# Performance work log

Hardware: AMD Instinct MI355X
Metric: run time of the kernel (lower is better)

## Reference

```python
import jax, jax.numpy as jnp
import numpy as np

DIM = 64
HEADS = 4            # self.num_heads = 2 * num_heads(=2)
SMK = 5
KS = 7
EPS = 1e-5
SCALE = (DIM // HEADS) ** -0.5


def pool_mat(n, out=7):
    # AdaptiveAvgPool2d bin matrix: P[i, j] = 1/size if floor(i*n/out) <= j < ceil((i+1)*n/out)
    P = np.zeros((out, n), np.float32)
    for i in range(out):
        s = (i * n) // out
        e = -((-(i + 1) * n) // out)
        P[i, s:e] = 1.0 / (e - s)
    return jnp.asarray(P)


def bn(x, g, b, m, v):
    # inference BatchNorm2d on [B,C,H,W]
    return (x - m[:, None, None]) * (g[:, None, None] * jax.lax.rsqrt(v[:, None, None] + EPS)) + b[:, None, None]


def conv1x1(x, w):
    return jnp.einsum('oi,bihw->bohw', w, x)


def rpb_bias(rpb, H, W, k):
    # replicate apply_rpb gather indexing (incl. the flip over flattened HW)
    rs = 2 * k - 1
    ih0 = np.arange(k)
    idx_k = (ih0[:, None] * rs + ih0[None, :]).reshape(-1)        # [k*k]
    rh = np.ones(k, np.int64); rh[k // 2] = H - (k - 1)
    rw = np.ones(k, np.int64); rw[k // 2] = W - (k - 1)
    ih = np.repeat(ih0, rh)                                       # [H]
    iw = np.repeat(ih0, rw)                                       # [W]
    bias_hw = ih[:, None] * rs + iw[None, :]                      # [H,W]
    bias_idx = (bias_hw[..., None] + idx_k).reshape(-1, k * k)[::-1].copy()  # [H*W,k*k]
    flat = rpb.reshape(rpb.shape[0], -1)                          # [G, rs*rs]
    return flat[:, bias_idx].reshape(1, rpb.shape[0], H, W, k * k)


def na2d_av(attn, value, k):
    # NATTEN-style neighborhood AV: window start clamped to stay in-bounds
    B, G, H, W, _ = attn.shape
    si = np.clip(np.arange(H) - k // 2, 0, H - k)
    sj = np.clip(np.arange(W) - k // 2, 0, W - k)
    ii = si[:, None] + np.arange(k)    # [H,k]
    jj = sj[:, None] + np.arange(k)    # [W,k]
    v = value[:, :, ii][:, :, :, :, jj]         # [B,G,H,k,W,k,C]
    a = attn.reshape(B, G, H, W, k, k)
    return jnp.einsum('bghwij,bghiwjc->bghwc', a, v)


def reference(x, wq_w, wq_g, wq_b, wq_m, wq_v,
              wk_w, wk_g, wk_b, wk_m, wk_v,
              proj_w, proj_b, rpb1, rpb2,
              dy_w, dy_g, dy_b, dy_m, dy_v):
    B, C, H, W = x.shape
    G = HEADS
    q, kctx = jnp.split(x, 2, axis=1)                      # [B,C/2,H,W] each
    q = bn(conv1x1(q, wq_w), wq_g, wq_b, wq_m, wq_v) * SCALE
    Ph, Pw = pool_mat(H), pool_mat(W)
    kp = jnp.einsum('ph,bchw,qw->bcpq', Ph, kctx, Pw)      # adaptive avg pool to 7x7
    k = bn(conv1x1(kp, wk_w), wk_g, wk_b, wk_m, wk_v)
    q = q.reshape(B, G, -1, H * W)                          # b g c n
    k = k.reshape(B, G, -1, 49)                             # b g c l
    w = jnp.einsum('bgcn,bgcl->bgnl', q, k)
    w = w.transpose(0, 3, 1, 2)                             # b l g n
    w = jnp.einsum('ol,blgn->bogn', proj_w, w) + proj_b[None, :, None, None]  # b (74) g n
    w = w.transpose(0, 2, 3, 1).reshape(B, G, H, W, SMK * SMK + KS * KS)
    attn1 = w[..., :SMK * SMK]
    attn2 = w[..., SMK * SMK:]
    attn1 = jax.nn.softmax(attn1 + rpb_bias(rpb1, H, W, SMK), axis=-1)
    attn2 = jax.nn.softmax(attn2 + rpb_bias(rpb2, H, W, KS), axis=-1)
    c = C // (2 * G)
    value = x.reshape(B, 2, G, c, H, W).transpose(1, 0, 2, 4, 5, 3)  # m b g h w c
    x1 = na2d_av(attn1, value[0], SMK)
    x2 = na2d_av(attn2, value[1], KS)
    out = jnp.concatenate([x1, x2], axis=1)                 # b (2g) h w c
    out = out.transpose(0, 1, 4, 2, 3).reshape(B, C, H, W)  # b (g c) h w
    return bn(conv1x1(out, dy_w), dy_g, dy_b, dy_m, dy_v)


def setup_inputs() -> dict:
    key = jax.random.key(0)
    ks = jax.random.split(key, 20)
    h = DIM // 2
    def bnp(k):
        k1, k2, k3, k4 = jax.random.split(k, 4)
        return (jax.random.uniform(k1, (0,)),)  # unused
    inp = {
        'x': jax.random.normal(ks[0], (8, DIM, 64, 64), jnp.float32),
        'wq_w': jax.random.normal(ks[1], (h, h), jnp.float32) * (h ** -0.5),
        'wq_g': jax.random.uniform(ks[2], (h,), jnp.float32, 0.5, 1.5),
        'wq_b': jax.random.normal(ks[3], (h,), jnp.float32) * 0.1,
        'wq_m': jax.random.normal(ks[4], (h,), jnp.float32) * 0.1,
        'wq_v': jax.random.uniform(ks[5], (h,), jnp.float32, 0.5, 1.5),
        'wk_w': jax.random.normal(ks[6], (h, h), jnp.float32) * (h ** -0.5),
        'wk_g': jax.random.uniform(ks[7], (h,), jnp.float32, 0.5, 1.5),
        'wk_b': jax.random.normal(ks[8], (h,), jnp.float32) * 0.1,
        'wk_m': jax.random.normal(ks[9], (h,), jnp.float32) * 0.1,
        'wk_v': jax.random.uniform(ks[10], (h,), jnp.float32, 0.5, 1.5),
        'proj_w': jax.random.normal(ks[11], (SMK * SMK + KS * KS, 49), jnp.float32) * (49 ** -0.5),
        'proj_b': jax.random.normal(ks[12], (SMK * SMK + KS * KS,), jnp.float32) * 0.02,
        'rpb1': jax.random.normal(ks[13], (HEADS, 2 * SMK - 1, 2 * SMK - 1), jnp.float32) * 0.02,
        'rpb2': jax.random.normal(ks[14], (HEADS, 2 * KS - 1, 2 * KS - 1), jnp.float32) * 0.02,
        'dy_w': jax.random.normal(ks[15], (DIM, DIM), jnp.float32) * (DIM ** -0.5),
        'dy_g': jax.random.uniform(ks[16], (DIM,), jnp.float32, 0.5, 1.5),
        'dy_b': jax.random.normal(ks[17], (DIM,), jnp.float32) * 0.1,
        'dy_m': jax.random.normal(ks[18], (DIM,), jnp.float32) * 0.1,
        'dy_v': jax.random.uniform(ks[19], (DIM,), jnp.float32, 0.5, 1.5),
    }
    return inp
```

## Files before the change

kernel.cpp:

```cpp
#include <hip/hip_runtime.h>

#define EPSV 1e-5f

#define OFF_W    12544
#define OFF_WQT  31488
#define OFF_DYT  32512

typedef float f4u __attribute__((ext_vector_type(4), aligned(4)));

__global__ __launch_bounds__(256) void pool_prep_kernel(
    const float* __restrict__ x,
    const float* __restrict__ wk_w, const float* __restrict__ wk_g,
    const float* __restrict__ wk_b, const float* __restrict__ wk_m,
    const float* __restrict__ wk_v,
    const float* __restrict__ wq_w, const float* __restrict__ dy_w,
    float* __restrict__ ws)
{
  const int bid = blockIdx.x;
  const int tid = threadIdx.x;

  if (bid >= 56) {
    const int t = (bid - 56) * 256 + tid;
    float* wqT = ws + OFF_WQT;
    float* dyT = ws + OFF_DYT;
    if (t < 1024) {
      const int i = t >> 5, o = t & 31;
      wqT[t] = wq_w[o * 32 + i];
    } else {
      const int t2 = t - 1024;
      const int i = t2 >> 6, o = t2 & 63;
      dyT[t2] = dy_w[o * 64 + i];
    }
    return;
  }

  float* kbuf = ws;
  const int b = bid / 7;
  const int p = bid % 7;
  __shared__ float s_tmp[32 * 64];
  __shared__ float s_kp[32 * 7];

  const int sh = (p * 64) / 7, eh = ((p + 1) * 64 + 6) / 7;
  const float invH = 1.0f / (float)(eh - sh);
  for (int idx = tid; idx < 2048; idx += 256) {
    const int c = idx >> 6, ww = idx & 63;
    const float* xp = x + ((size_t)(b * 64 + 32 + c)) * 4096 + ww;
    float s = 0.f;
    for (int hh = sh; hh < eh; ++hh) s += xp[hh * 64];
    s_tmp[idx] = s * invH;
  }
  __syncthreads();
  if (tid < 224) {
    const int c = tid / 7, q = tid % 7;
    const int sw = (q * 64) / 7, ew = ((q + 1) * 64 + 6) / 7;
    float s = 0.f;
    for (int ww = sw; ww < ew; ++ww) s += s_tmp[c * 64 + ww];
    s_kp[c * 7 + q] = s / (float)(ew - sw);
  }
  __syncthreads();
  if (tid < 224) {
    const int o = tid / 7, q = tid % 7;
    float s = 0.f;
#pragma unroll
    for (int i = 0; i < 32; i++) s += wk_w[o * 32 + i] * s_kp[i * 7 + q];
    const float sc = wk_g[o] * rsqrtf(wk_v[o] + EPSV);
    const int g = o >> 3, c = o & 7, l = p * 7 + q;
    kbuf[(((size_t)b * 4 + g) * 8 + c) * 49 + l] =
        (s - wk_m[o]) * sc + wk_b[o];
  }
}

__global__ __launch_bounds__(256) void fold_w_kernel(
    const float* __restrict__ proj_w, const float* __restrict__ ws_in,
    float* __restrict__ Wout)
{
  const int bg = blockIdx.x;
  const int tid = threadIdx.x;
  __shared__ float s_k[392];
  for (int i = tid; i < 392; i += 256) s_k[i] = ws_in[(size_t)bg * 392 + i];
  __syncthreads();
  for (int idx = tid; idx < 592; idx += 256) {
    const int o = idx >> 3, c = idx & 7;
    float s = 0.f;
#pragma unroll
    for (int l = 0; l < 49; l++) s += proj_w[o * 49 + l] * s_k[c * 49 + l];
    Wout[(size_t)bg * 592 + idx] = s;
  }
}

__global__ __launch_bounds__(512, 3) void contmix_main(
    const float* __restrict__ x,
    const float* __restrict__ wq_g, const float* __restrict__ wq_b,
    const float* __restrict__ wq_m, const float* __restrict__ wq_v,
    const float* __restrict__ proj_b,
    const float* __restrict__ rpb1, const float* __restrict__ rpb2,
    const float* __restrict__ dy_g, const float* __restrict__ dy_b,
    const float* __restrict__ dy_m, const float* __restrict__ dy_v,
    const float* __restrict__ ws,
    float* __restrict__ out)
{
  __shared__ float s_rpb1[4 * 81];
  __shared__ float s_rpb2[4 * 169];
  __shared__ float s_val[64 * 64];
  __shared__ float s_q[32 * 64];

  const int bx = blockIdx.x;
  const int b = bx >> 6;
  const int h = bx & 63;
  const int tid = threadIdx.x;
  const int w = tid & 63;
  const int bru = __builtin_amdgcn_readfirstlane(tid >> 8);
  const int gu  = __builtin_amdgcn_readfirstlane((tid >> 6) & 3);

  for (int i = tid; i < 324; i += 512) s_rpb1[i] = rpb1[i];
  for (int i = tid; i < 676; i += 512) s_rpb2[i] = rpb2[i];

  const float* xb = x + (size_t)b * 64 * 4096;

  float q8[8];
  if (bru == 0) {
#pragma unroll
    for (int o = 0; o < 8; o++) q8[o] = 0.f;
    const float* wqt = ws + OFF_WQT + gu * 8;
#pragma unroll
    for (int i = 0; i < 32; i++) {
      const float xv = xb[i * 4096 + h * 64 + w];
#pragma unroll
      for (int o = 0; o < 8; o++) q8[o] += wqt[i * 32 + o] * xv;
    }
#pragma unroll
    for (int o = 0; o < 8; o++) {
      const int oc = gu * 8 + o;
      const float s = wq_g[oc] * rsqrtf(wq_v[oc] + EPSV);
      q8[o] = (q8[o] * s + (wq_b[oc] - wq_m[oc] * s)) * 0.25f;
      s_q[(gu * 8 + o) * 64 + w] = q8[o];
    }
  }
  __syncthreads();
  if (bru != 0) {
#pragma unroll
    for (int o = 0; o < 8; o++) q8[o] = s_q[(gu * 8 + o) * 64 + w];
  }

  const float* Wr = ws + OFF_W + (size_t)(b * 4 + gu) * 592;

  const int ph = 63 - h, pw = 63 - w;

  if (bru == 0) {
    const int bih5 = ph - min(max(ph - 2, 0), 59);
    const int biw5 = pw - min(max(pw - 2, 0), 59);
    const int si5 = min(max(h - 2, 0), 59), sj5 = min(max(w - 2, 0), 59);
    float l1[25];
#pragma unroll
    for (int o = 0; o < 25; o++) {
      const float* wo = Wr + o * 8;
      float s = proj_b[o];
#pragma unroll
      for (int c = 0; c < 8; c++) s += wo[c] * q8[c];
      l1[o] = s;
    }
    const float* rp1 = s_rpb1 + gu * 81 + bih5 * 9 + biw5;
#pragma unroll
    for (int ki = 0; ki < 5; ki++)
#pragma unroll
      for (int kj = 0; kj < 5; kj++) l1[ki * 5 + kj] += rp1[ki * 9 + kj];

    float mx = l1[0];
#pragma unroll
    for (int o = 1; o < 25; o++) mx = fmaxf(mx, l1[o]);
    float sum = 0.f;
#pragma unroll
    for (int o = 0; o < 25; o++) {
      const float e = __expf(l1[o] - mx);
      l1[o] = e;
      sum += e;
    }
    const float inv = 1.f / sum;

    float acc[8];
#pragma unroll
    for (int c = 0; c < 8; c++) acc[c] = 0.f;
    const float* vb = xb + gu * 8 * 4096;
#pragma unroll
    for (int i = 0; i < 5; i++) {
      const float a0 = l1[i * 5 + 0], a1 = l1[i * 5 + 1], a2 = l1[i * 5 + 2];
      const float a3 = l1[i * 5 + 3], a4 = l1[i * 5 + 4];
      const float* vr0 = vb + (si5 + i) * 64 + sj5;
#pragma unroll
      for (int c = 0; c < 8; c++) {
        const float* vr = vr0 + c * 4096;
        const f4u f = *(const f4u*)vr;
        const float v4 = vr[4];
        acc[c] += a0 * f.x + a1 * f.y + a2 * f.z + a3 * f.w + a4 * v4;
      }
    }
#pragma unroll
    for (int c = 0; c < 8; c++) s_val[(gu * 8 + c) * 64 + w] = acc[c] * inv;
  } else {
    const int bih7 = ph - min(max(ph - 3, 0), 57);
    const int biw7 = pw - min(max(pw - 3, 0), 57);
    const int si7 = min(max(h - 3, 0), 57), sj7 = min(max(w - 3, 0), 57);
    float l2[49];
#pragma unroll
    for (int o = 0; o < 49; o++) {
      const float* wo = Wr + (25 + o) * 8;
      float s = proj_b[25 + o];
#pragma unroll
      for (int c = 0; c < 8; c++) s += wo[c] * q8[c];
      l2[o] = s;
    }
    const float* rp2 = s_rpb2 + gu * 169 + bih7 * 13 + biw7;
#pragma unroll
    for (int ki = 0; ki < 7; ki++)
#pragma unroll
      for (int kj = 0; kj < 7; kj++) l2[ki * 7 + kj] += rp2[ki * 13 + kj];

    float mx = l2[0];
#pragma unroll
    for (int o = 1; o < 49; o++) mx = fmaxf(mx, l2[o]);
    float sum = 0.f;
#pragma unroll
    for (int o = 0; o < 49; o++) {
      const float e = __expf(l2[o] - mx);
      l2[o] = e;
      sum += e;
    }
    const float inv = 1.f / sum;

    float acc[8];
#pragma unroll
    for (int c = 0; c < 8; c++) acc[c] = 0.f;
    const float* vb = xb + (32 + gu * 8) * 4096;
#pragma unroll
    for (int i = 0; i < 7; i++) {
      const float a0 = l2[i * 7 + 0], a1 = l2[i * 7 + 1], a2 = l2[i * 7 + 2];
      const float a3 = l2[i * 7 + 3], a4 = l2[i * 7 + 4], a5 = l2[i * 7 + 5];
      const float a6 = l2[i * 7 + 6];
      const float* vr0 = vb + (si7 + i) * 64 + sj7;
#pragma unroll
      for (int c = 0; c < 8; c++) {
        const float* vr = vr0 + c * 4096;
        const f4u fa = *(const f4u*)vr;
        const f4u fb = *(const f4u*)(vr + 3);
        acc[c] += a0 * fa.x + a1 * fa.y + a2 * fa.z + a3 * fa.w +
                  a4 * fb.y + a5 * fb.z + a6 * fb.w;
      }
    }
#pragma unroll
    for (int c = 0; c < 8; c++) s_val[(32 + gu * 8 + c) * 64 + w] = acc[c] * inv;
  }

  __syncthreads();

  {
    const int ogu = __builtin_amdgcn_readfirstlane(tid >> 6);
    float facc[8];
#pragma unroll
    for (int oo = 0; oo < 8; oo++) facc[oo] = 0.f;
    const float* dyt = ws + OFF_DYT + ogu * 8;
#pragma unroll
    for (int i = 0; i < 64; i++) {
      const float v = s_val[i * 64 + w];
#pragma unroll
      for (int oo = 0; oo < 8; oo++) facc[oo] += dyt[i * 64 + oo] * v;
    }
#pragma unroll
    for (int oo = 0; oo < 8; oo++) {
      const int oc = ogu * 8 + oo;
      const float sc = dy_g[oc] * rsqrtf(dy_v[oc] + EPSV);
      out[((size_t)(b * 64 + oc)) * 4096 + h * 64 + w] =
          (facc[oo] - dy_m[oc]) * sc + dy_b[oc];
    }
  }
}

extern "C" void kernel_launch(void* const* d_in, const int* in_sizes, int n_in,
                              void* d_out, int out_size, void* d_ws, size_t ws_size,
                              hipStream_t stream)
{
  const float* x      = (const float*)d_in[0];
  const float* wq_w   = (const float*)d_in[1];
  const float* wq_g   = (const float*)d_in[2];
  const float* wq_b   = (const float*)d_in[3];
  const float* wq_m   = (const float*)d_in[4];
  const float* wq_v   = (const float*)d_in[5];
  const float* wk_w   = (const float*)d_in[6];
  const float* wk_g   = (const float*)d_in[7];
  const float* wk_b   = (const float*)d_in[8];
  const float* wk_m   = (const float*)d_in[9];
  const float* wk_v   = (const float*)d_in[10];
  const float* proj_w = (const float*)d_in[11];
  const float* proj_b = (const float*)d_in[12];
  const float* rpb1   = (const float*)d_in[13];
  const float* rpb2   = (const float*)d_in[14];
  const float* dy_w   = (const float*)d_in[15];
  const float* dy_g   = (const float*)d_in[16];
  const float* dy_b   = (const float*)d_in[17];
  const float* dy_m   = (const float*)d_in[18];
  const float* dy_v   = (const float*)d_in[19];

  float* ws = (float*)d_ws;

  pool_prep_kernel<<<76, 256, 0, stream>>>(x, wk_w, wk_g, wk_b, wk_m, wk_v,
                                           wq_w, dy_w, ws);
  fold_w_kernel<<<32, 256, 0, stream>>>(proj_w, ws, ws + OFF_W);
  contmix_main<<<512, 512, 0, stream>>>(x, wq_g, wq_b, wq_m, wq_v,
                                        proj_b, rpb1, rpb2,
                                        dy_g, dy_b, dy_m, dy_v,
                                        ws, (float*)d_out);
}
```

Baseline: 170.0 us.

## Split fused attention kernel into per-branch blocks plus separate final conv

Splits the fused main kernel in two. The first kernel runs the 5x5 and 7x7 attention branches in separate 256-thread blocks (1024 blocks), each recomputing q from an LDS-staged x row, and writes the attended values to a global workspace buffer. The second kernel loads those values into LDS and applies the final 1x1 conv with BatchNorm. The goal is to remove load imbalance between the 25-tap and 49-tap branches within a block and to drop register pressure. The cost is an extra kernel launch, a global round trip for the intermediate values, and duplicated q computation.

```diff
diff --git a/kernel.cpp b/kernel.cpp
--- a/kernel.cpp
+++ b/kernel.cpp
@@ -5,6 +5,7 @@
 #define OFF_W    12544
 #define OFF_WQT  31488
 #define OFF_DYT  32512
+#define OFF_VAL  40960
 
 typedef float f4u __attribute__((ext_vector_type(4), aligned(4)));
 
@@ -88,43 +89,47 @@
   }
 }
 
-__global__ __launch_bounds__(512, 3) void contmix_main(
+__global__ __launch_bounds__(256) void attn_kernel(
     const float* __restrict__ x,
     const float* __restrict__ wq_g, const float* __restrict__ wq_b,
     const float* __restrict__ wq_m, const float* __restrict__ wq_v,
     const float* __restrict__ proj_b,
     const float* __restrict__ rpb1, const float* __restrict__ rpb2,
-    const float* __restrict__ dy_g, const float* __restrict__ dy_b,
-    const float* __restrict__ dy_m, const float* __restrict__ dy_v,
     const float* __restrict__ ws,
-    float* __restrict__ out)
-{
-  __shared__ float s_rpb1[4 * 81];
-  __shared__ float s_rpb2[4 * 169];
-  __shared__ float s_val[64 * 64];
-  __shared__ float s_q[32 * 64];
-
-  const int bx = blockIdx.x;
-  const int b = bx >> 6;
-  const int h = bx & 63;
+    float* __restrict__ vbuf)
+{
+  __shared__ float s_rpb[4 * 169];
+  __shared__ float s_xq[32 * 64];
+
+  const int bid = blockIdx.x;
+  const int br = bid & 1;
+  const int h = (bid >> 1) & 63;
+  const int b = bid >> 7;
   const int tid = threadIdx.x;
   const int w = tid & 63;
-  const int bru = __builtin_amdgcn_readfirstlane(tid >> 8);
-  const int gu  = __builtin_amdgcn_readfirstlane((tid >> 6) & 3);
-
-  for (int i = tid; i < 324; i += 512) s_rpb1[i] = rpb1[i];
-  for (int i = tid; i < 676; i += 512) s_rpb2[i] = rpb2[i];
+  const int gu = __builtin_amdgcn_readfirstlane(tid >> 6);
 
   const float* xb = x + (size_t)b * 64 * 4096;
 
+  for (int idx = tid; idx < 2048; idx += 256) {
+    const int c = idx >> 6, ww = idx & 63;
+    s_xq[idx] = xb[c * 4096 + h * 64 + ww];
+  }
+  if (br == 0) {
+    for (int i = tid; i < 324; i += 256) s_rpb[i] = rpb1[i];
+  } else {
+    for (int i = tid; i < 676; i += 256) s_rpb[i] = rpb2[i];
+  }
+  __syncthreads();
+
   float q8[8];
-  if (bru == 0) {
-#pragma unroll
-    for (int o = 0; o < 8; o++) q8[o] = 0.f;
+#pragma unroll
+  for (int o = 0; o < 8; o++) q8[o] = 0.f;
+  {
     const float* wqt = ws + OFF_WQT + gu * 8;
 #pragma unroll
     for (int i = 0; i < 32; i++) {
-      const float xv = xb[i * 4096 + h * 64 + w];
+      const float xv = s_xq[i * 64 + w];
 #pragma unroll
       for (int o = 0; o < 8; o++) q8[o] += wqt[i * 32 + o] * xv;
     }
@@ -133,20 +138,14 @@
       const int oc = gu * 8 + o;
       const float s = wq_g[oc] * rsqrtf(wq_v[oc] + EPSV);
       q8[o] = (q8[o] * s + (wq_b[oc] - wq_m[oc] * s)) * 0.25f;
-      s_q[(gu * 8 + o) * 64 + w] = q8[o];
-    }
-  }
-  __syncthreads();
-  if (bru != 0) {
-#pragma unroll
-    for (int o = 0; o < 8; o++) q8[o] = s_q[(gu * 8 + o) * 64 + w];
+    }
   }
 
   const float* Wr = ws + OFF_W + (size_t)(b * 4 + gu) * 592;
 
   const int ph = 63 - h, pw = 63 - w;
 
-  if (bru == 0) {
+  if (br == 0) {
     const int bih5 = ph - min(max(ph - 2, 0), 59);
     const int biw5 = pw - min(max(pw - 2, 0), 59);
     const int si5 = min(max(h - 2, 0), 59), sj5 = min(max(w - 2, 0), 59);
@@ -159,7 +158,7 @@
       for (int c = 0; c < 8; c++) s += wo[c] * q8[c];
       l1[o] = s;
     }
-    const float* rp1 = s_rpb1 + gu * 81 + bih5 * 9 + biw5;
+    const float* rp1 = s_rpb + gu * 81 + bih5 * 9 + biw5;
 #pragma unroll
     for (int ki = 0; ki < 5; ki++)
 #pragma unroll
@@ -195,7 +194,8 @@
       }
     }
 #pragma unroll
-    for (int c = 0; c < 8; c++) s_val[(gu * 8 + c) * 64 + w] = acc[c] * inv;
+    for (int c = 0; c < 8; c++)
+      vbuf[((size_t)(b * 64 + gu * 8 + c)) * 4096 + h * 64 + w] = acc[c] * inv;
   } else {
     const int bih7 = ph - min(max(ph - 3, 0), 57);
     const int biw7 = pw - min(max(pw - 3, 0), 57);
@@ -209,7 +209,7 @@
       for (int c = 0; c < 8; c++) s += wo[c] * q8[c];
       l2[o] = s;
     }
-    const float* rp2 = s_rpb2 + gu * 169 + bih7 * 13 + biw7;
+    const float* rp2 = s_rpb + gu * 169 + bih7 * 13 + biw7;
 #pragma unroll
     for (int ki = 0; ki < 7; ki++)
 #pragma unroll
@@ -247,30 +247,51 @@
       }
     }
 #pragma unroll
-    for (int c = 0; c < 8; c++) s_val[(32 + gu * 8 + c) * 64 + w] = acc[c] * inv;
-  }
-
-  __syncthreads();
-
-  {
-    const int ogu = __builtin_amdgcn_readfirstlane(tid >> 6);
-    float facc[8];
-#pragma unroll
-    for (int oo = 0; oo < 8; oo++) facc[oo] = 0.f;
-    const float* dyt = ws + OFF_DYT + ogu * 8;
-#pragma unroll
-    for (int i = 0; i < 64; i++) {
-      const float v = s_val[i * 64 + w];
-#pragma unroll
-      for (int oo = 0; oo < 8; oo++) facc[oo] += dyt[i * 64 + oo] * v;
-    }
-#pragma unroll
-    for (int oo = 0; oo < 8; oo++) {
-      const int oc = ogu * 8 + oo;
-      const float sc = dy_g[oc] * rsqrtf(dy_v[oc] + EPSV);
-      out[((size_t)(b * 64 + oc)) * 4096 + h * 64 + w] =
-          (facc[oo] - dy_m[oc]) * sc + dy_b[oc];
-    }
+    for (int c = 0; c < 8; c++)
+      vbuf[((size_t)(b * 64 + 32 + gu * 8 + c)) * 4096 + h * 64 + w] =
+          acc[c] * inv;
+  }
+}
+
+__global__ __launch_bounds__(512) void final_conv_kernel(
+    const float* __restrict__ vbuf,
+    const float* __restrict__ dy_g, const float* __restrict__ dy_b,
+    const float* __restrict__ dy_m, const float* __restrict__ dy_v,
+    const float* __restrict__ ws,
+    float* __restrict__ out)
+{
+  __shared__ float s_val[64 * 64];
+
+  const int bx = blockIdx.x;
+  const int b = bx >> 6;
+  const int h = bx & 63;
+  const int tid = threadIdx.x;
+  const int w = tid & 63;
+  const int ogu = __builtin_amdgcn_readfirstlane(tid >> 6);
+
+  for (int idx4 = tid; idx4 < 1024; idx4 += 512) {
+    const int ic = idx4 >> 4, w4 = idx4 & 15;
+    *(f4u*)&s_val[ic * 64 + w4 * 4] =
+        *(const f4u*)&vbuf[((size_t)(b * 64 + ic)) * 4096 + h * 64 + w4 * 4];
+  }
+  __syncthreads();
+
+  float facc[8];
+#pragma unroll
+  for (int oo = 0; oo < 8; oo++) facc[oo] = 0.f;
+  const float* dyt = ws + OFF_DYT + ogu * 8;
+#pragma unroll
+  for (int i = 0; i < 64; i++) {
+    const float v = s_val[i * 64 + w];
+#pragma unroll
+    for (int oo = 0; oo < 8; oo++) facc[oo] += dyt[i * 64 + oo] * v;
+  }
+#pragma unroll
+  for (int oo = 0; oo < 8; oo++) {
+    const int oc = ogu * 8 + oo;
+    const float sc = dy_g[oc] * rsqrtf(dy_v[oc] + EPSV);
+    out[((size_t)(b * 64 + oc)) * 4096 + h * 64 + w] =
+        (facc[oo] - dy_m[oc]) * sc + dy_b[oc];
   }
 }
 
@@ -304,8 +325,10 @@
   pool_prep_kernel<<<76, 256, 0, stream>>>(x, wk_w, wk_g, wk_b, wk_m, wk_v,
                                            wq_w, dy_w, ws);
   fold_w_kernel<<<32, 256, 0, stream>>>(proj_w, ws, ws + OFF_W);
-  contmix_main<<<512, 512, 0, stream>>>(x, wq_g, wq_b, wq_m, wq_v,
+  attn_kernel<<<1024, 256, 0, stream>>>(x, wq_g, wq_b, wq_m, wq_v,
                                         proj_b, rpb1, rpb2,
-                                        dy_g, dy_b, dy_m, dy_v,
-                                        ws, (float*)d_out);
-}
+                                        ws, ws + OFF_VAL);
+  final_conv_kernel<<<512, 512, 0, stream>>>(ws + OFF_VAL,
+                                             dy_g, dy_b, dy_m, dy_v,
+                                             ws, (float*)d_out);
+}
```

Measured after the change: 196.8 us. 15.8% more time.

## Recompute q in every wave, tree-reduce softmax, raise occupancy bound

Applied to the files above, without the earlier changes.

Every half of the block now computes the q projection redundantly instead of one half computing it and sharing through LDS, which removes the s_q buffer and one barrier dependency. The max and sum reductions in both softmaxes become pairwise trees to shorten dependency chains. Launch bounds are raised to 4 blocks per CU. In exchange, the redundant q work doubles global reads of x for q, and the tighter register cap could cause spills.

```diff
diff --git a/kernel.cpp b/kernel.cpp
--- a/kernel.cpp
+++ b/kernel.cpp
@@ -7,6 +7,37 @@
 #define OFF_DYT  32512
 
 typedef float f4u __attribute__((ext_vector_type(4), aligned(4)));
+
+#define FMAXOP(a, b) fmaxf((a), (b))
+#define FADDOP(a, b) ((a) + (b))
+
+#define TREE25(op, arr, res)                                         \
+  {                                                                  \
+    float u_[13];                                                    \
+    _Pragma("unroll") for (int i_ = 0; i_ < 12; i_++)                \
+        u_[i_] = op(arr[i_], arr[i_ + 12]);                          \
+    u_[12] = arr[24];                                                \
+    _Pragma("unroll") for (int i_ = 0; i_ < 6; i_++)                 \
+        u_[i_] = op(u_[i_], u_[i_ + 6]);                             \
+    _Pragma("unroll") for (int i_ = 0; i_ < 3; i_++)                 \
+        u_[i_] = op(u_[i_], u_[i_ + 3]);                             \
+    res = op(op(op(u_[0], u_[1]), u_[2]), u_[12]);                   \
+  }
+
+#define TREE49(op, arr, res)                                         \
+  {                                                                  \
+    float u_[25];                                                    \
+    _Pragma("unroll") for (int i_ = 0; i_ < 24; i_++)                \
+        u_[i_] = op(arr[i_], arr[i_ + 24]);                          \
+    u_[24] = arr[48];                                                \
+    _Pragma("unroll") for (int i_ = 0; i_ < 12; i_++)                \
+        u_[i_] = op(u_[i_], u_[i_ + 12]);                            \
+    _Pragma("unroll") for (int i_ = 0; i_ < 6; i_++)                 \
+        u_[i_] = op(u_[i_], u_[i_ + 6]);                             \
+    _Pragma("unroll") for (int i_ = 0; i_ < 3; i_++)                 \
+        u_[i_] = op(u_[i_], u_[i_ + 3]);                             \
+    res = op(op(op(u_[0], u_[1]), u_[2]), u_[24]);                   \
+  }
 
 __global__ __launch_bounds__(256) void pool_prep_kernel(
     const float* __restrict__ x,
@@ -88,7 +119,7 @@
   }
 }
 
-__global__ __launch_bounds__(512, 3) void contmix_main(
+__global__ __launch_bounds__(512, 4) void contmix_main(
     const float* __restrict__ x,
     const float* __restrict__ wq_g, const float* __restrict__ wq_b,
     const float* __restrict__ wq_m, const float* __restrict__ wq_v,
@@ -102,7 +133,6 @@
   __shared__ float s_rpb1[4 * 81];
   __shared__ float s_rpb2[4 * 169];
   __shared__ float s_val[64 * 64];
-  __shared__ float s_q[32 * 64];
 
   const int bx = blockIdx.x;
   const int b = bx >> 6;
@@ -114,13 +144,14 @@
 
   for (int i = tid; i < 324; i += 512) s_rpb1[i] = rpb1[i];
   for (int i = tid; i < 676; i += 512) s_rpb2[i] = rpb2[i];
+  __syncthreads();
 
   const float* xb = x + (size_t)b * 64 * 4096;
 
   float q8[8];
-  if (bru == 0) {
-#pragma unroll
-    for (int o = 0; o < 8; o++) q8[o] = 0.f;
+#pragma unroll
+  for (int o = 0; o < 8; o++) q8[o] = 0.f;
+  {
     const float* wqt = ws + OFF_WQT + gu * 8;
 #pragma unroll
     for (int i = 0; i < 32; i++) {
@@ -133,13 +164,7 @@
       const int oc = gu * 8 + o;
       const float s = wq_g[oc] * rsqrtf(wq_v[oc] + EPSV);
       q8[o] = (q8[o] * s + (wq_b[oc] - wq_m[oc] * s)) * 0.25f;
-      s_q[(gu * 8 + o) * 64 + w] = q8[o];
-    }
-  }
-  __syncthreads();
-  if (bru != 0) {
-#pragma unroll
-    for (int o = 0; o < 8; o++) q8[o] = s_q[(gu * 8 + o) * 64 + w];
+    }
   }
 
   const float* Wr = ws + OFF_W + (size_t)(b * 4 + gu) * 592;
@@ -165,16 +190,12 @@
 #pragma unroll
       for (int kj = 0; kj < 5; kj++) l1[ki * 5 + kj] += rp1[ki * 9 + kj];
 
-    float mx = l1[0];
-#pragma unroll
-    for (int o = 1; o < 25; o++) mx = fmaxf(mx, l1[o]);
-    float sum = 0.f;
-#pragma unroll
-    for (int o = 0; o < 25; o++) {
-      const float e = __expf(l1[o] - mx);
-      l1[o] = e;
-      sum += e;
-    }
+    float mx;
+    TREE25(FMAXOP, l1, mx);
+#pragma unroll
+    for (int o = 0; o < 25; o++) l1[o] = __expf(l1[o] - mx);
+    float sum;
+    TREE25(FADDOP, l1, sum);
     const float inv = 1.f / sum;
 
     float acc[8];
@@ -215,16 +236,12 @@
 #pragma unroll
       for (int kj = 0; kj < 7; kj++) l2[ki * 7 + kj] += rp2[ki * 13 + kj];
 
-    float mx = l2[0];
-#pragma unroll
-    for (int o = 1; o < 49; o++) mx = fmaxf(mx, l2[o]);
-    float sum = 0.f;
-#pragma unroll
-    for (int o = 0; o < 49; o++) {
-      const float e = __expf(l2[o] - mx);
-      l2[o] = e;
-      sum += e;
-    }
+    float mx;
+    TREE49(FMAXOP, l2, mx);
+#pragma unroll
+    for (int o = 0; o < 49; o++) l2[o] = __expf(l2[o] - mx);
+    float sum;
+    TREE49(FADDOP, l2, sum);
     const float inv = 1.f / sum;
 
     float acc[8];
```

New measurement: 165.8 us. 2.5% less time.
